# Kernel optimization log

Measured on AMD Instinct MI355X. Metric: run time of the kernel, lower is better.

## Reference

```python
import jax, jax.numpy as jnp
import numpy as np

B, FEAT, SPD_H, CTRL_H, N_CMD = 32768, 512, 128, 256, 4


def _p(key, shape, fan_in):
    # torch nn.Linear default init: U(-1/sqrt(fan_in), 1/sqrt(fan_in))
    lim = 1.0 / np.sqrt(fan_in)
    return jax.random.uniform(key, shape, jnp.float32, -lim, lim)


def setup_inputs() -> dict:
    key = jax.random.key(0)
    ks = iter(jax.random.split(key, 32))
    inp = {
        "feat": jax.random.normal(next(ks), (B, FEAT), jnp.float32),
        "speed": jax.random.uniform(next(ks), (B,), jnp.float32),
        "command": jax.random.randint(next(ks), (B,), 0, N_CMD, jnp.int32),
        "ms_w1": _p(next(ks), (1, SPD_H), 1), "ms_b1": _p(next(ks), (SPD_H,), 1),
        "ms_w2": _p(next(ks), (SPD_H, SPD_H), SPD_H), "ms_b2": _p(next(ks), (SPD_H,), SPD_H),
        "ms_w3": _p(next(ks), (SPD_H, SPD_H), SPD_H), "ms_b3": _p(next(ks), (SPD_H,), SPD_H),
        # speed_pred_module: 512 -> 256 -> 256 -> 1
        "sp_w1": _p(next(ks), (FEAT, CTRL_H), FEAT), "sp_b1": _p(next(ks), (CTRL_H,), FEAT),
        "sp_w2": _p(next(ks), (CTRL_H, CTRL_H), CTRL_H), "sp_b2": _p(next(ks), (CTRL_H,), CTRL_H),
        "sp_w3": _p(next(ks), (CTRL_H, 1), CTRL_H), "sp_b3": _p(next(ks), (1,), CTRL_H),
        # join_module: Linear(640, 512)
        "join_w": _p(next(ks), (FEAT + SPD_H, FEAT), FEAT + SPD_H),
        "join_b": _p(next(ks), (FEAT,), FEAT + SPD_H),
        # 4 control heads: 512 -> 256 -> 256 -> 3 (stacked on expert axis e)
        "ctrl_w1": _p(next(ks), (N_CMD, FEAT, CTRL_H), FEAT), "ctrl_b1": _p(next(ks), (N_CMD, CTRL_H), FEAT),
        "ctrl_w2": _p(next(ks), (N_CMD, CTRL_H, CTRL_H), CTRL_H), "ctrl_b2": _p(next(ks), (N_CMD, CTRL_H), CTRL_H),
        "ctrl_w3": _p(next(ks), (N_CMD, CTRL_H, 3), CTRL_H), "ctrl_b3": _p(next(ks), (N_CMD, 3), CTRL_H),
    }
    return inp


def _mlp(x, w1, b1, w2, b2, w3, b3):
    # FullyConnectedNet: Linear, ReLU, Linear, Dropout(p=0 -> noop), ReLU, Linear
    h = jax.nn.relu(x @ w1 + b1)
    h = jax.nn.relu(h @ w2 + b2)
    return h @ w3 + b3


def reference(feat, speed, command,
              ms_w1, ms_b1, ms_w2, ms_b2, ms_w3, ms_b3,
              sp_w1, sp_b1, sp_w2, sp_b2, sp_w3, sp_b3,
              join_w, join_b,
              ctrl_w1, ctrl_b1, ctrl_w2, ctrl_b2, ctrl_w3, ctrl_b3):
    v = _mlp(speed[:, None], ms_w1, ms_b1, ms_w2, ms_b2, ms_w3, ms_b3)      # [B,128]
    joined = jnp.concatenate([feat, v], axis=1) @ join_w + join_b           # [B,512]
    v_p = _mlp(feat, sp_w1, sp_b1, sp_w2, sp_b2, sp_w3, sp_b3)              # [B,1]
    # command-indexed dispatch: compute all 4 heads densely, then select per sample
    h1 = jax.nn.relu(jnp.einsum('bd,edh->beh', joined, ctrl_w1) + ctrl_b1)  # [B,4,256]
    h2 = jax.nn.relu(jnp.einsum('beh,ehk->bek', h1, ctrl_w2) + ctrl_b2)     # [B,4,256]
    act_all = jnp.einsum('bek,eko->beo', h2, ctrl_w3) + ctrl_b3             # [B,4,3]
    action = jnp.take_along_axis(act_all, command[:, None, None].astype(jnp.int32), axis=1)[:, 0]  # [B,3]
    throttle = jax.nn.sigmoid(action[:, 0])
    steering = jnp.tanh(action[:, 1])
    brake = jax.nn.sigmoid(action[:, 2])
    return v_p, throttle, brake, steering
```

## Files before the change

### kernel.cpp

```cpp
#include <hip/hip_runtime.h>
#include <hip/hip_bf16.h>
#include <stdint.h>
#include <math.h>

#define BB 32768
#define FEAT 512
#define SPD_H 128
#define CTRL_H 256
#define NCMD 4

typedef __attribute__((ext_vector_type(8))) short bf16x8;
typedef __attribute__((ext_vector_type(4))) float f32x4;

__device__ __forceinline__ unsigned short f2bf(float f) {
  union { float f; uint32_t u; } v; v.f = f;
  uint32_t u = v.u;
  return (unsigned short)((u + 0x7fffu + ((u >> 16) & 1u)) >> 16);
}

__device__ __forceinline__ void async16(const unsigned short* g, unsigned short* l) {
  __builtin_amdgcn_global_load_lds(
      (const __attribute__((address_space(1))) unsigned int*)g,
      (__attribute__((address_space(3))) unsigned int*)l, 16, 0, 0);
}

__device__ __forceinline__ void gemm128(
    const unsigned short* __restrict__ A, int lda,
    const int* __restrict__ perm, int m_start, int m_cnt,
    const unsigned short* __restrict__ W, const float* __restrict__ bi,
    unsigned short* __restrict__ C, int ldc, int relu, int K, int mt, int nt) {
  extern __shared__ __align__(16) unsigned char dynsm[];
  unsigned short* As = (unsigned short*)dynsm;
  unsigned short* Bs = As + 128 * 32;

  const int m0 = mt * 128;
  if (m0 >= m_cnt) return;
  const int n0 = nt * 128;
  const int t = threadIdx.x;
  const int w = t >> 6, lane = t & 63;
  const int wm = w & 1, wn = w >> 1;

  f32x4 acc[4][4];
#pragma unroll
  for (int i = 0; i < 4; ++i)
#pragma unroll
    for (int j = 0; j < 4; ++j)
#pragma unroll
      for (int r = 0; r < 4; ++r) acc[i][j][r] = 0.f;

  const int fr = lane & 15;
  const int fk = (lane >> 4) * 8;

  const unsigned short* agp[2]; const unsigned short* bgp[2];
  unsigned short* al[2]; unsigned short* bl[2];
#pragma unroll
  for (int it = 0; it < 2; ++it) {
    int row = w * 32 + it * 16 + (lane >> 2);
    int seg8 = (lane & 3) * 8;
    int rl = m0 + row;
    if (rl >= m_cnt) rl = m_cnt - 1;
    int grow = perm ? perm[m_start + rl] : (m_start + rl);
    agp[it] = A + (size_t)grow * lda + seg8;
    bgp[it] = W + (size_t)(n0 + row) * K + seg8;
    al[it] = As + (w * 32 + it * 16) * 32;
    bl[it] = Bs + (w * 32 + it * 16) * 32;
  }

  for (int k0 = 0; k0 < K; k0 += 32) {
#pragma unroll
    for (int it = 0; it < 2; ++it) {
      async16(agp[it] + k0, al[it]);
      async16(bgp[it] + k0, bl[it]);
    }
    __syncthreads();
    bf16x8 af[4], bfv[4];
#pragma unroll
    for (int i = 0; i < 4; ++i)
      af[i] = *(const bf16x8*)(As + (wm * 64 + i * 16 + fr) * 32 + fk);
#pragma unroll
    for (int j = 0; j < 4; ++j)
      bfv[j] = *(const bf16x8*)(Bs + (wn * 64 + j * 16 + fr) * 32 + fk);
#pragma unroll
    for (int i = 0; i < 4; ++i)
#pragma unroll
      for (int j = 0; j < 4; ++j)
        acc[i][j] = __builtin_amdgcn_mfma_f32_16x16x32_bf16(af[i], bfv[j], acc[i][j], 0, 0, 0);
    __syncthreads();
  }

  const int rquad = (lane >> 4) * 4;
  const int cidx = lane & 15;

  float bv[4];
#pragma unroll
  for (int j = 0; j < 4; ++j) bv[j] = bi ? bi[n0 + wn * 64 + j * 16 + cidx] : 0.f;

  unsigned short (*bscr)[136] = (unsigned short(*)[136])dynsm;
#pragma unroll
  for (int c = 0; c < 4; ++c) {
    if (wm == (c >> 1)) {
#pragma unroll
      for (int j = 0; j < 4; ++j) {
#pragma unroll
        for (int ii = 0; ii < 2; ++ii) {
          int i = 2 * (c & 1) + ii;
          int lr = ii * 16 + rquad;
#pragma unroll
          for (int r = 0; r < 4; ++r) {
            float v = acc[i][j][r] + bv[j];
            if (relu) v = fmaxf(v, 0.f);
            bscr[lr + r][wn * 64 + j * 16 + cidx] = f2bf(v);
          }
        }
      }
    }
    __syncthreads();
#pragma unroll
    for (int q = 0; q < 2; ++q) {
      int sg = t + 256 * q;
      int lr = sg >> 4, cs = (sg & 15) * 8;
      int grow = m0 + c * 32 + lr;
      if (grow < m_cnt)
        *(bf16x8*)(C + (size_t)(m_start + grow) * ldc + (n0 + cs)) =
            *(const bf16x8*)(&bscr[lr][cs]);
    }
    __syncthreads();
  }
}

struct WSeg { const float* src; unsigned short* dst; int K; int N; int ldd; };
struct PrepArgs {
  WSeg s[12];
  int start[13];
  const float* join_w; unsigned short* wjbf;
  const float* feat; unsigned short* ajoin;
  const int* cmd; int* wavecnt;
  const float* join_b; const float* ctrl_w1; const float* ctrl_b1; float* b_f;
};
__launch_bounds__(256)
__global__ void k_prep(PrepArgs a) {
  int bx = blockIdx.x, t = threadIdx.x;
  if (bx < 16384) {
    int idx = bx * 256 + t;
    int i = idx >> 7;
    int j4 = (idx & 127) << 2;
    float4 f = *(const float4*)(a.feat + (size_t)i * FEAT + j4);
    ushort4 o;
    o.x = f2bf(f.x); o.y = f2bf(f.y); o.z = f2bf(f.z); o.w = f2bf(f.w);
    *(ushort4*)(a.ajoin + (size_t)i * 640 + j4) = o;
    return;
  }
  int rel = bx - 16384;
  if (rel < 320) {
    int idx = rel * 256 + t;
    float4 f = *(const float4*)(a.join_w + (size_t)idx * 4);
    ushort4 o;
    o.x = f2bf(f.x); o.y = f2bf(f.y); o.z = f2bf(f.z); o.w = f2bf(f.w);
    *(ushort4*)(a.wjbf + (size_t)idx * 4) = o;
    return;
  }
  rel -= 320;
  if (rel < a.start[12]) {
    __shared__ float tb[32][33];
    int si = 0;
    while (rel >= a.start[si + 1]) ++si;
    WSeg sg = a.s[si];
    int tile = rel - a.start[si];
    int tkx = sg.K >> 5;
    int tn = tile / tkx;
    int tk = tile - tn * tkx;
    int k0 = tk * 32, n0 = tn * 32;
    int tx = t & 31, ty = t >> 5;
#pragma unroll
    for (int j = 0; j < 4; ++j)
      tb[ty + j * 8][tx] = sg.src[(size_t)(k0 + ty + j * 8) * sg.N + n0 + tx];
    __syncthreads();
#pragma unroll
    for (int j = 0; j < 4; ++j)
      sg.dst[(size_t)(n0 + ty + j * 8) * sg.ldd + k0 + tx] = f2bf(tb[tx][ty + j * 8]);
    return;
  }
  rel -= a.start[12];
  if (rel < 128) {
    int i = rel * 256 + t;
    int c = a.cmd[i];
    int wid = i >> 6;
    int lane = t & 63;
#pragma unroll
    for (int cv = 0; cv < NCMD; ++cv) {
      unsigned long long m = __ballot(c == cv);
      if (lane == 0) a.wavecnt[cv * 512 + wid] = __popcll(m);
    }
    return;
  }
  int e = rel - 128;
  float s0 = a.ctrl_b1[e * 256 + t], s1 = 0.f, s2 = 0.f, s3 = 0.f;
  const float* w = a.ctrl_w1 + (size_t)e * 512 * 256 + t;
#pragma unroll 4
  for (int m = 0; m < 512; m += 4) {
    s0 = fmaf(a.join_b[m + 0], w[(size_t)(m + 0) * 256], s0);
    s1 = fmaf(a.join_b[m + 1], w[(size_t)(m + 1) * 256], s1);
    s2 = fmaf(a.join_b[m + 2], w[(size_t)(m + 2) * 256], s2);
    s3 = fmaf(a.join_b[m + 3], w[(size_t)(m + 3) * 256], s3);
  }
  a.b_f[e * 256 + t] = (s0 + s1) + (s2 + s3);
}

struct MidArgs {
  const int* cmd; const int* wavecnt; int* perm; int* offs;
  const unsigned short* c_w1t; const unsigned short* wjbf; unsigned short* wf_t;
  const float* speed;
  const float* ms_w1; const float* ms_b1;
  const unsigned short* ms_w2t; const float* ms_b2;
  const unsigned short* ms_w3t; const float* ms_b3;
  unsigned short* ajoin;
  int* tile_e; int* tile_r0; int* ntl;
};
__launch_bounds__(256)
__global__ void k_mid(MidArgs a) {
  int b = blockIdx.x, t = threadIdx.x;
  if (b >= 168) {
    extern __shared__ __align__(16) unsigned char dynsm[];
    unsigned short (*hw)[136] = (unsigned short(*)[136])dynsm;
    unsigned short* BsM = (unsigned short*)(dynsm + 128 * 136 * 2);
    const int m0 = (b - 168) * 128;
    const int w = t >> 6, lane = t & 63;
    const int wm = w & 1, wn = w >> 1;
    const int fr = lane & 15, fk = (lane >> 4) * 8;
    const int rquad = (lane >> 4) * 4, cidx = lane & 15;
    {
      int r = t >> 1, half = t & 1;
      float s = a.speed[m0 + r];
#pragma unroll
      for (int c0 = 0; c0 < 64; c0 += 4) {
        int c = half * 64 + c0;
        float4 wv = *(const float4*)(a.ms_w1 + c);
        float4 bv = *(const float4*)(a.ms_b1 + c);
        hw[r][c + 0] = f2bf(fmaxf(fmaf(s, wv.x, bv.x), 0.f));
        hw[r][c + 1] = f2bf(fmaxf(fmaf(s, wv.y, bv.y), 0.f));
        hw[r][c + 2] = f2bf(fmaxf(fmaf(s, wv.z, bv.z), 0.f));
        hw[r][c + 3] = f2bf(fmaxf(fmaf(s, wv.w, bv.w), 0.f));
      }
    }
    __syncthreads();
    for (int layer = 0; layer < 2; ++layer) {
      const unsigned short* Wt = layer ? a.ms_w3t : a.ms_w2t;
      const float* bb = layer ? a.ms_b3 : a.ms_b2;
      f32x4 acc[4][4];
#pragma unroll
      for (int i = 0; i < 4; ++i)
#pragma unroll
        for (int j = 0; j < 4; ++j)
#pragma unroll
          for (int r = 0; r < 4; ++r) acc[i][j][r] = 0.f;
      for (int k0 = 0; k0 < 128; k0 += 32) {
#pragma unroll
        for (int it = 0; it < 2; ++it) {
          int row = w * 32 + it * 16 + (lane >> 2);
          async16(Wt + (size_t)row * 128 + k0 + (lane & 3) * 8,
                  BsM + (w * 32 + it * 16) * 32);
        }
        __syncthreads();
        bf16x8 af[4], bfv[4];
#pragma unroll
        for (int i = 0; i < 4; ++i)
          af[i] = *(const bf16x8*)(&hw[wm * 64 + i * 16 + fr][k0 + fk]);
#pragma unroll
        for (int j = 0; j < 4; ++j)
          bfv[j] = *(const bf16x8*)(BsM + (wn * 64 + j * 16 + fr) * 32 + fk);
#pragma unroll
        for (int i = 0; i < 4; ++i)
#pragma unroll
          for (int j = 0; j < 4; ++j)
            acc[i][j] = __builtin_amdgcn_mfma_f32_16x16x32_bf16(af[i], bfv[j], acc[i][j], 0, 0, 0);
        __syncthreads();
      }
#pragma unroll
      for (int j = 0; j < 4; ++j) {
        int col = wn * 64 + j * 16 + cidx;
        float bv = bb[col];
#pragma unroll
        for (int i = 0; i < 4; ++i) {
          int row = wm * 64 + i * 16 + rquad;
#pragma unroll
          for (int r = 0; r < 4; ++r) {
            float v = acc[i][j][r] + bv;
            if (layer == 0) v = fmaxf(v, 0.f);
            hw[row + r][col] = f2bf(v);
          }
        }
      }
      __syncthreads();
    }
    {
      int r = t >> 1, half = t & 1;
#pragma unroll
      for (int c8 = 0; c8 < 8; ++c8)
        *(bf16x8*)(a.ajoin + (size_t)(m0 + r) * 640 + 512 + half * 64 + c8 * 8) =
            *(const bf16x8*)(&hw[r][half * 64 + c8 * 8]);
    }
    return;
  }
  if (b >= 128) {
    int idx = b - 128;
    int mt = idx & 7, nt = idx >> 3;
    gemm128(a.c_w1t, 512, nullptr, 0, 1024, a.wjbf, nullptr, a.wf_t, 640, 0, 512, mt, nt);
    return;
  }
  __shared__ int pf[NCMD][4];
  __shared__ int tot[NCMD];
  int c = t >> 6, lane = t & 63;
  int v[8]; int s = 0;
#pragma unroll
  for (int q = 0; q < 8; ++q) { v[q] = a.wavecnt[c * 512 + lane * 8 + q]; s += v[q]; }
  int p = s;
#pragma unroll
  for (int m = 1; m < 64; m <<= 1) { int o = __shfl_up(p, m, 64); if (lane >= m) p += o; }
  int excl = p - s;
  if (lane == 63) tot[c] = p;
  if (lane == ((4 * b) >> 3)) {
    int base_off = (4 * b) & 7;
    int run = excl;
#pragma unroll
    for (int q = 0; q < 8; ++q) {
      if (q >= base_off && q < base_off + 4) pf[c][q - base_off] = run;
      run += v[q];
    }
  }
  __syncthreads();
  int soffs[NCMD + 1];
  soffs[0] = 0;
#pragma unroll
  for (int e = 0; e < NCMD; ++e) soffs[e + 1] = soffs[e] + tot[e];
  if (b == 0 && t == 0)
    for (int e = 0; e <= NCMD; ++e) a.offs[e] = soffs[e];
  int i = b * 256 + t;
  int mc = a.cmd[i];
  int lwid = t >> 6;
  int rank = 0, base = 0;
#pragma unroll
  for (int cv = 0; cv < NCMD; ++cv) {
    unsigned long long m = __ballot(mc == cv);
    if (mc == cv) {
      rank = __popcll(m & ((1ull << lane) - 1ull));
      base = soffs[cv] + pf[cv][lwid];
    }
  }
  a.perm[base + rank] = i;

  if (b == 0) {
    int toff[NCMD + 1];
    toff[0] = 0;
#pragma unroll
    for (int ee = 0; ee < NCMD; ++ee) toff[ee + 1] = toff[ee] + ((tot[ee] + 63) >> 6);
    if (t == 0) a.ntl[0] = toff[NCMD];
    for (int ti = t; ti < toff[NCMD]; ti += 256) {
      int ee = 0;
      while (ti >= toff[ee + 1]) ++ee;
      a.tile_e[ti] = ee;
      a.tile_r0[ti] = soffs[ee] + (ti - toff[ee]) * 64;
    }
  }
}

struct TailArgs {
  const unsigned short* ajoin;
  const unsigned short* wf_t;  const float* b_f;
  const unsigned short* sp_w1t; const float* sp_b1;
  const unsigned short* c_w2t; const float* ctrl_b2;
  const unsigned short* sp_w2t; const float* sp_b2;
  const float* ctrl_w3; const float* ctrl_b3;
  const float* sp_w3; const float* sp_b3;
  const int* perm; const int* seg;
  const int* tile_e; const int* tile_r0; const int* ntl;
  float* out;
};
__launch_bounds__(256, 3)
__global__ void k_tail(TailArgs a) {
  extern __shared__ __align__(16) unsigned char dynsm[];
  unsigned short* As = (unsigned short*)dynsm;
  unsigned short* h1 = (unsigned short*)(dynsm + 16384);
  float* pscr = (float*)dynsm;

  const int t = threadIdx.x;
  const int w = t >> 6, lane = t & 63;
  const int fr = lane & 15, fcg = lane >> 4;
  const int rquad = fcg * 4, cidx = fr;
  const int fkS = ((fcg ^ (fr & 3)) << 3);

  int is_sp, e = 0, NC;
  const unsigned short *W1, *W2;
  const float *b1, *b2;
  int r0, rend;
  if (blockIdx.x < 512) {
    is_sp = 1; NC = 8;
    W1 = a.sp_w1t; W2 = a.sp_w2t; b1 = a.sp_b1; b2 = a.sp_b2;
    r0 = blockIdx.x * 64; rend = BB;
  } else {
    int ti = blockIdx.x - 512;
    if (ti >= a.ntl[0]) return;
    is_sp = 0; e = a.tile_e[ti]; NC = 10;
    W1 = a.wf_t + (size_t)e * 256 * 640;
    W2 = a.c_w2t + (size_t)e * 65536;
    b1 = a.b_f + e * 256; b2 = a.ctrl_b2 + e * 256;
    r0 = a.tile_r0[ti]; rend = a.seg[e + 1];
  }
  const int K = is_sp ? 512 : 640;

  const unsigned short* agp[2];
  {
    int rl = r0 + w * 16 + (lane >> 2);
    if (rl >= rend) rl = rend - 1;
    int grow = is_sp ? rl : a.perm[rl];
    const unsigned short* g0 =
        a.ajoin + (size_t)grow * 640 + (((lane & 3) ^ ((lane >> 2) & 3)) << 3);
    agp[0] = g0; agp[1] = g0 + 32;
  }
  unsigned short* alb0 = As + w * 16 * 32;
  unsigned short* alb1 = As + 2048 + w * 16 * 32;

  const unsigned short* bp[4];
#pragma unroll
  for (int j = 0; j < 4; ++j)
    bp[j] = W1 + (size_t)(w * 64 + j * 16 + fr) * K + fcg * 8;

  f32x4 acc[4][4];
#pragma unroll
  for (int i = 0; i < 4; ++i)
#pragma unroll
    for (int j = 0; j < 4; ++j)
#pragma unroll
      for (int r = 0; r < 4; ++r) acc[i][j][r] = 0.f;

  async16(agp[0], alb0);
  async16(agp[1], alb1);

  for (int c = 0; c < NC; ++c) {
    const int cur = (c & 1) * 4096;
    if (c + 1 < NC) {
      const int nb = ((c + 1) & 1) * 4096;
      async16(agp[0] + (c + 1) * 64, alb0 + nb);
      async16(agp[1] + (c + 1) * 64, alb1 + nb);
      asm volatile("s_waitcnt vmcnt(2)" ::: "memory");
    } else {
      asm volatile("s_waitcnt vmcnt(0)" ::: "memory");
    }
    __builtin_amdgcn_s_barrier();
#pragma unroll
    for (int ks = 0; ks < 2; ++ks) {
      const int k0 = c * 64 + ks * 32;
      bf16x8 af[4], bv[4];
#pragma unroll
      for (int i = 0; i < 4; ++i)
        af[i] = *(const bf16x8*)(As + cur + ks * 2048 + (i * 16 + fr) * 32 + fkS);
#pragma unroll
      for (int j = 0; j < 4; ++j)
        bv[j] = *(const bf16x8*)(bp[j] + k0);
#pragma unroll
      for (int i = 0; i < 4; ++i)
#pragma unroll
        for (int j = 0; j < 4; ++j)
          acc[i][j] = __builtin_amdgcn_mfma_f32_16x16x32_bf16(af[i], bv[j], acc[i][j], 0, 0, 0);
    }
    __builtin_amdgcn_s_barrier();
  }

#pragma unroll
  for (int j = 0; j < 4; ++j) {
    const int col = w * 64 + j * 16 + cidx;
    const float bj = b1[col];
    const int c8 = col >> 3, cl = col & 7;
#pragma unroll
    for (int i = 0; i < 4; ++i) {
#pragma unroll
      for (int r = 0; r < 4; ++r) {
        const int row = i * 16 + rquad + r;
        h1[(row << 8) + (((c8 ^ (row & 7)) << 3) | cl)] =
            f2bf(fmaxf(acc[i][j][r] + bj, 0.f));
      }
    }
  }
  __syncthreads();

  const unsigned short* bp2[4];
#pragma unroll
  for (int j = 0; j < 4; ++j)
    bp2[j] = W2 + (size_t)(w * 64 + j * 16 + fr) * 256 + fcg * 8;

#pragma unroll
  for (int i = 0; i < 4; ++i)
#pragma unroll
    for (int j = 0; j < 4; ++j)
#pragma unroll
      for (int r = 0; r < 4; ++r) acc[i][j][r] = 0.f;

#pragma unroll 2
  for (int k0 = 0; k0 < 256; k0 += 32) {
    bf16x8 af[4], bv[4];
#pragma unroll
    for (int i = 0; i < 4; ++i) {
      const int row = i * 16 + fr;
      const int c8 = (k0 >> 3) + fcg;
      af[i] = *(const bf16x8*)(h1 + (row << 8) + ((c8 ^ (row & 7)) << 3));
    }
#pragma unroll
    for (int j = 0; j < 4; ++j)
      bv[j] = *(const bf16x8*)(bp2[j] + k0);
#pragma unroll
    for (int i = 0; i < 4; ++i)
#pragma unroll
      for (int j = 0; j < 4; ++j)
        acc[i][j] = __builtin_amdgcn_mfma_f32_16x16x32_bf16(af[i], bv[j], acc[i][j], 0, 0, 0);
  }

  float b2v[4], w30[4], w31[4], w32[4];
#pragma unroll
  for (int j = 0; j < 4; ++j) {
    const int col = w * 64 + j * 16 + cidx;
    b2v[j] = b2[col];
    if (is_sp) {
      w30[j] = a.sp_w3[col]; w31[j] = 0.f; w32[j] = 0.f;
    } else {
      const float* wp = a.ctrl_w3 + (size_t)e * 768 + col * 3;
      w30[j] = wp[0]; w31[j] = wp[1]; w32[j] = wp[2];
    }
  }
#pragma unroll
  for (int i = 0; i < 4; ++i) {
#pragma unroll
    for (int r = 0; r < 4; ++r) {
      float s0 = 0.f, s1 = 0.f, s2 = 0.f;
#pragma unroll
      for (int j = 0; j < 4; ++j) {
        const float v = fmaxf(acc[i][j][r] + b2v[j], 0.f);
        s0 = fmaf(v, w30[j], s0);
        if (!is_sp) { s1 = fmaf(v, w31[j], s1); s2 = fmaf(v, w32[j], s2); }
      }
#pragma unroll
      for (int m = 1; m <= 8; m <<= 1) {
        s0 += __shfl_xor(s0, m, 64);
        if (!is_sp) { s1 += __shfl_xor(s1, m, 64); s2 += __shfl_xor(s2, m, 64); }
      }
      if (cidx == 0) {
        const int row = i * 16 + rquad + r;
        pscr[(row * 4 + w) * 3 + 0] = s0;
        if (!is_sp) {
          pscr[(row * 4 + w) * 3 + 1] = s1;
          pscr[(row * 4 + w) * 3 + 2] = s2;
        }
      }
    }
  }
  __syncthreads();

  if (is_sp) {
    if (t < 64) {
      float s = pscr[t * 12] + pscr[t * 12 + 3] + pscr[t * 12 + 6] + pscr[t * 12 + 9]
              + a.sp_b3[0];
      a.out[r0 + t] = s;
    }
  } else {
    if (t < 192) {
      const int row = t / 3, o = t - row * 3;
      const int rl = r0 + row;
      if (rl < rend) {
        float s = pscr[row * 12 + o] + pscr[row * 12 + 3 + o] +
                  pscr[row * 12 + 6 + o] + pscr[row * 12 + 9 + o] +
                  a.ctrl_b3[e * 3 + o];
        const int orig = a.perm[rl];
        if (o == 0)      a.out[BB + orig]     = 1.f / (1.f + __expf(-s));
        else if (o == 2) a.out[2 * BB + orig] = 1.f / (1.f + __expf(-s));
        else             a.out[3 * BB + orig] = tanhf(s);
      }
    }
  }
}

static inline size_t align256(size_t x) { return (x + 255) & ~(size_t)255; }

extern "C" void kernel_launch(void* const* d_in, const int* in_sizes, int n_in,
                              void* d_out, int out_size, void* d_ws, size_t ws_size,
                              hipStream_t stream) {
  const float* feat   = (const float*)d_in[0];
  const float* speed  = (const float*)d_in[1];
  const int*   command= (const int*)d_in[2];
  const float* ms_w1  = (const float*)d_in[3];
  const float* ms_b1  = (const float*)d_in[4];
  const float* ms_w2  = (const float*)d_in[5];
  const float* ms_b2  = (const float*)d_in[6];
  const float* ms_w3  = (const float*)d_in[7];
  const float* ms_b3  = (const float*)d_in[8];
  const float* sp_w1  = (const float*)d_in[9];
  const float* sp_b1  = (const float*)d_in[10];
  const float* sp_w2  = (const float*)d_in[11];
  const float* sp_b2  = (const float*)d_in[12];
  const float* sp_w3  = (const float*)d_in[13];
  const float* sp_b3  = (const float*)d_in[14];
  const float* join_w = (const float*)d_in[15];
  const float* join_b = (const float*)d_in[16];
  const float* ctrl_w1= (const float*)d_in[17];
  const float* ctrl_b1= (const float*)d_in[18];
  const float* ctrl_w2= (const float*)d_in[19];
  const float* ctrl_b2= (const float*)d_in[20];
  const float* ctrl_w3= (const float*)d_in[21];
  const float* ctrl_b3= (const float*)d_in[22];
  float* out = (float*)d_out;

  char* ws = (char*)d_ws;
  size_t off = 0;
  auto alloc = [&](size_t bytes) -> char* { char* p = ws + off; off = align256(off + bytes); return p; };

  unsigned short* ajoin  = (unsigned short*)alloc((size_t)BB * 640 * 2);
  unsigned short* wtp    = (unsigned short*)alloc(1998848ull * 2);
  int* perm    = (int*)alloc((size_t)BB * 4);
  int* cnt     = (int*)alloc(64);
  int* wavecnt = (int*)alloc(4 * 512 * 4);
  float* b_f   = (float*)alloc(4 * 256 * 4);
  int* tile_e  = (int*)alloc(520 * 4);
  int* tile_r0 = (int*)alloc(520 * 4);
  int* ntl     = (int*)alloc(64);

  unsigned short* sp_w1t = wtp;
  unsigned short* sp_w2t = wtp + 131072;
  unsigned short* ms_w2t = wtp + 196608;
  unsigned short* ms_w3t = wtp + 212992;
  unsigned short* c_w1t  = wtp + 229376;
  unsigned short* c_w2t  = wtp + 753664;
  unsigned short* wjbf   = wtp + 1015808;
  unsigned short* wf_t   = wtp + 1343488;

  PrepArgs P;
  P.s[0] = { sp_w1, sp_w1t, 512, 256, 512 };
  P.s[1] = { sp_w2, sp_w2t, 256, 256, 256 };
  P.s[2] = { ms_w2, ms_w2t, 128, 128, 128 };
  P.s[3] = { ms_w3, ms_w3t, 128, 128, 128 };
  for (int e = 0; e < 4; ++e) P.s[4 + e] = { ctrl_w1 + (size_t)e * 512 * 256, c_w1t + (size_t)e * 131072, 512, 256, 512 };
  for (int e = 0; e < 4; ++e) P.s[8 + e] = { ctrl_w2 + (size_t)e * 256 * 256, c_w2t + (size_t)e * 65536, 256, 256, 256 };
  P.start[0] = 0;
  for (int i = 0; i < 12; ++i)
    P.start[i + 1] = P.start[i] + (P.s[i].K >> 5) * (P.s[i].N >> 5);
  P.join_w = join_w; P.wjbf = wjbf;
  P.feat = feat; P.ajoin = ajoin;
  P.cmd = command; P.wavecnt = wavecnt;
  P.join_b = join_b; P.ctrl_w1 = ctrl_w1; P.ctrl_b1 = ctrl_b1; P.b_f = b_f;
  int prep_blocks = 16384 + 320 + P.start[12] + 128 + 4;

  k_prep<<<prep_blocks, 256, 0, stream>>>(P);

  MidArgs Mi;
  Mi.cmd = command; Mi.wavecnt = wavecnt; Mi.perm = perm; Mi.offs = cnt + 4;
  Mi.c_w1t = c_w1t; Mi.wjbf = wjbf; Mi.wf_t = wf_t;
  Mi.speed = speed;
  Mi.ms_w1 = ms_w1; Mi.ms_b1 = ms_b1;
  Mi.ms_w2t = ms_w2t; Mi.ms_b2 = ms_b2;
  Mi.ms_w3t = ms_w3t; Mi.ms_b3 = ms_b3;
  Mi.ajoin = ajoin;
  Mi.tile_e = tile_e; Mi.tile_r0 = tile_r0; Mi.ntl = ntl;
  k_mid<<<168 + 256, 256, 128 * 136 * 2 + 128 * 32 * 2, stream>>>(Mi);

  TailArgs T;
  T.ajoin = ajoin; T.wf_t = wf_t; T.b_f = b_f;
  T.sp_w1t = sp_w1t; T.sp_b1 = sp_b1;
  T.c_w2t = c_w2t; T.ctrl_b2 = ctrl_b2;
  T.sp_w2t = sp_w2t; T.sp_b2 = sp_b2;
  T.ctrl_w3 = ctrl_w3; T.ctrl_b3 = ctrl_b3;
  T.sp_w3 = sp_w3; T.sp_b3 = sp_b3;
  T.perm = perm; T.seg = cnt + 4;
  T.tile_e = tile_e; T.tile_r0 = tile_r0; T.ntl = ntl;
  T.out = out;
  k_tail<<<dim3(512 + 516), 256, 49152, stream>>>(T);
}
```

Measured before the change: 240.7 us.

## Fuse speed-pred and control heads into one 512-thread tile sharing A loads

The tail kernel now runs both the speed-prediction MLP and the command-selected control head in the same 512-thread block. Waves 0-3 handle control and waves 4-7 handle speed-pred, and both consume one shared 64-wide swizzled A tile of permuted joined rows. This removes the separate 512 speed-pred blocks and their duplicate reads of the feature rows. Speed-pred outputs are scattered back through the permutation. The fused-bias precompute is also split across 32 blocks with partial sums, reduced by 4 extra blocks in the mid kernel, trading an extra pass for more parallelism. The cost is higher LDS use (80KB) and idle speed-pred waves during the extra K chunks.

```diff
diff --git a/kernel.cpp b/kernel.cpp
--- a/kernel.cpp
+++ b/kernel.cpp
@@ -135,7 +135,7 @@
   const float* join_w; unsigned short* wjbf;
   const float* feat; unsigned short* ajoin;
   const int* cmd; int* wavecnt;
-  const float* join_b; const float* ctrl_w1; const float* ctrl_b1; float* b_f;
+  const float* join_b; const float* ctrl_w1; float* bf_part;
 };
 __launch_bounds__(256)
 __global__ void k_prep(PrepArgs a) {
@@ -193,17 +193,25 @@
     }
     return;
   }
-  int e = rel - 128;
-  float s0 = a.ctrl_b1[e * 256 + t], s1 = 0.f, s2 = 0.f, s3 = 0.f;
-  const float* w = a.ctrl_w1 + (size_t)e * 512 * 256 + t;
-#pragma unroll 4
-  for (int m = 0; m < 512; m += 4) {
-    s0 = fmaf(a.join_b[m + 0], w[(size_t)(m + 0) * 256], s0);
-    s1 = fmaf(a.join_b[m + 1], w[(size_t)(m + 1) * 256], s1);
-    s2 = fmaf(a.join_b[m + 2], w[(size_t)(m + 2) * 256], s2);
-    s3 = fmaf(a.join_b[m + 3], w[(size_t)(m + 3) * 256], s3);
-  }
-  a.b_f[e * 256 + t] = (s0 + s1) + (s2 + s3);
+  int idx = rel - 128;
+  int e = idx >> 3, ch = idx & 7;
+  const float* w = a.ctrl_w1 + (size_t)e * 512 * 256 + (size_t)ch * 64 * 256 + t;
+  const float* jb = a.join_b + ch * 64;
+  float s0 = 0.f, s1 = 0.f, s2 = 0.f, s3 = 0.f;
+  float s4 = 0.f, s5 = 0.f, s6 = 0.f, s7 = 0.f;
+#pragma unroll
+  for (int g = 0; g < 8; ++g) {
+    s0 = fmaf(jb[g * 8 + 0], w[(size_t)(g * 8 + 0) * 256], s0);
+    s1 = fmaf(jb[g * 8 + 1], w[(size_t)(g * 8 + 1) * 256], s1);
+    s2 = fmaf(jb[g * 8 + 2], w[(size_t)(g * 8 + 2) * 256], s2);
+    s3 = fmaf(jb[g * 8 + 3], w[(size_t)(g * 8 + 3) * 256], s3);
+    s4 = fmaf(jb[g * 8 + 4], w[(size_t)(g * 8 + 4) * 256], s4);
+    s5 = fmaf(jb[g * 8 + 5], w[(size_t)(g * 8 + 5) * 256], s5);
+    s6 = fmaf(jb[g * 8 + 6], w[(size_t)(g * 8 + 6) * 256], s6);
+    s7 = fmaf(jb[g * 8 + 7], w[(size_t)(g * 8 + 7) * 256], s7);
+  }
+  a.bf_part[(size_t)(e * 8 + ch) * 256 + t] =
+      ((s0 + s1) + (s2 + s3)) + ((s4 + s5) + (s6 + s7));
 }
 
 struct MidArgs {
@@ -214,11 +222,20 @@
   const unsigned short* ms_w2t; const float* ms_b2;
   const unsigned short* ms_w3t; const float* ms_b3;
   unsigned short* ajoin;
+  const float* bf_part; const float* ctrl_b1; float* b_f;
   int* tile_e; int* tile_r0; int* ntl;
 };
 __launch_bounds__(256)
 __global__ void k_mid(MidArgs a) {
   int b = blockIdx.x, t = threadIdx.x;
+  if (b >= 424) {
+    int e = b - 424;
+    float s = a.ctrl_b1[e * 256 + t];
+#pragma unroll
+    for (int ch = 0; ch < 8; ++ch) s += a.bf_part[(size_t)(e * 8 + ch) * 256 + t];
+    a.b_f[e * 256 + t] = s;
+    return;
+  }
   if (b >= 168) {
     extern __shared__ __align__(16) unsigned char dynsm[];
     unsigned short (*hw)[136] = (unsigned short(*)[136])dynsm;
@@ -375,54 +392,51 @@
   const int* tile_e; const int* tile_r0; const int* ntl;
   float* out;
 };
-__launch_bounds__(256, 3)
+__launch_bounds__(512, 4)
 __global__ void k_tail(TailArgs a) {
   extern __shared__ __align__(16) unsigned char dynsm[];
-  unsigned short* As = (unsigned short*)dynsm;
-  unsigned short* h1 = (unsigned short*)(dynsm + 16384);
-  float* pscr = (float*)dynsm;
+  unsigned short* As  = (unsigned short*)dynsm;
+  unsigned short* h1c = (unsigned short*)(dynsm + 16384);
+  unsigned short* h1s = (unsigned short*)(dynsm + 49152);
+  float* pscr_c = (float*)dynsm;
+  float* pscr_s = (float*)(dynsm + 4096);
 
   const int t = threadIdx.x;
-  const int w = t >> 6, lane = t & 63;
+  const int wv = t >> 6, lane = t & 63;
   const int fr = lane & 15, fcg = lane >> 4;
   const int rquad = fcg * 4, cidx = fr;
-  const int fkS = ((fcg ^ (fr & 3)) << 3);
-
-  int is_sp, e = 0, NC;
-  const unsigned short *W1, *W2;
-  const float *b1, *b2;
-  int r0, rend;
-  if (blockIdx.x < 512) {
-    is_sp = 1; NC = 8;
-    W1 = a.sp_w1t; W2 = a.sp_w2t; b1 = a.sp_b1; b2 = a.sp_b2;
-    r0 = blockIdx.x * 64; rend = BB;
+
+  const int ti = blockIdx.x;
+  if (ti >= a.ntl[0]) return;
+  const int e = a.tile_e[ti];
+  const int r0 = a.tile_r0[ti], rend = a.seg[e + 1];
+
+  const bool is_sp = wv >= 4;
+  const int w = wv & 3;
+
+  int srow = r0 + wv * 8 + (lane >> 3);
+  if (srow >= rend) srow = rend - 1;
+  const unsigned short* asrc =
+      a.ajoin + (size_t)a.perm[srow] * 640 + (((lane & 7) ^ (lane >> 3)) << 3);
+  unsigned short* sdst = As + wv * 512;
+
+  const unsigned short* W1; const float* b1;
+  const unsigned short* W2; const float* b2;
+  unsigned short* h1;
+  int K1, NCm;
+  if (is_sp) {
+    W1 = a.sp_w1t; b1 = a.sp_b1; W2 = a.sp_w2t; b2 = a.sp_b2;
+    h1 = h1s; K1 = 512; NCm = 8;
   } else {
-    int ti = blockIdx.x - 512;
-    if (ti >= a.ntl[0]) return;
-    is_sp = 0; e = a.tile_e[ti]; NC = 10;
-    W1 = a.wf_t + (size_t)e * 256 * 640;
-    W2 = a.c_w2t + (size_t)e * 65536;
-    b1 = a.b_f + e * 256; b2 = a.ctrl_b2 + e * 256;
-    r0 = a.tile_r0[ti]; rend = a.seg[e + 1];
-  }
-  const int K = is_sp ? 512 : 640;
-
-  const unsigned short* agp[2];
-  {
-    int rl = r0 + w * 16 + (lane >> 2);
-    if (rl >= rend) rl = rend - 1;
-    int grow = is_sp ? rl : a.perm[rl];
-    const unsigned short* g0 =
-        a.ajoin + (size_t)grow * 640 + (((lane & 3) ^ ((lane >> 2) & 3)) << 3);
-    agp[0] = g0; agp[1] = g0 + 32;
-  }
-  unsigned short* alb0 = As + w * 16 * 32;
-  unsigned short* alb1 = As + 2048 + w * 16 * 32;
+    W1 = a.wf_t + (size_t)e * 256 * 640; b1 = a.b_f + e * 256;
+    W2 = a.c_w2t + (size_t)e * 65536; b2 = a.ctrl_b2 + e * 256;
+    h1 = h1c; K1 = 640; NCm = 10;
+  }
 
   const unsigned short* bp[4];
 #pragma unroll
   for (int j = 0; j < 4; ++j)
-    bp[j] = W1 + (size_t)(w * 64 + j * 16 + fr) * K + fcg * 8;
+    bp[j] = W1 + (size_t)(w * 64 + j * 16 + fr) * K1 + fcg * 8;
 
   f32x4 acc[4][4];
 #pragma unroll
@@ -432,37 +446,35 @@
 #pragma unroll
       for (int r = 0; r < 4; ++r) acc[i][j][r] = 0.f;
 
-  async16(agp[0], alb0);
-  async16(agp[1], alb1);
-
-  for (int c = 0; c < NC; ++c) {
-    const int cur = (c & 1) * 4096;
-    if (c + 1 < NC) {
-      const int nb = ((c + 1) & 1) * 4096;
-      async16(agp[0] + (c + 1) * 64, alb0 + nb);
-      async16(agp[1] + (c + 1) * 64, alb1 + nb);
-      asm volatile("s_waitcnt vmcnt(2)" ::: "memory");
-    } else {
-      asm volatile("s_waitcnt vmcnt(0)" ::: "memory");
-    }
-    __builtin_amdgcn_s_barrier();
-#pragma unroll
-    for (int ks = 0; ks < 2; ++ks) {
-      const int k0 = c * 64 + ks * 32;
-      bf16x8 af[4], bv[4];
-#pragma unroll
-      for (int i = 0; i < 4; ++i)
-        af[i] = *(const bf16x8*)(As + cur + ks * 2048 + (i * 16 + fr) * 32 + fkS);
-#pragma unroll
-      for (int j = 0; j < 4; ++j)
-        bv[j] = *(const bf16x8*)(bp[j] + k0);
-#pragma unroll
-      for (int i = 0; i < 4; ++i)
+  async16(asrc, sdst);
+  async16(asrc + 64, sdst + 4096);
+
+  for (int c = 0; c < 10; ++c) {
+    if (c < 9) asm volatile("s_waitcnt vmcnt(1)" ::: "memory");
+    else       asm volatile("s_waitcnt vmcnt(0)" ::: "memory");
+    asm volatile("s_barrier" ::: "memory");
+    if (c < NCm) {
+      const unsigned short* cbuf = As + (c & 1) * 4096;
+#pragma unroll
+      for (int ks = 0; ks < 2; ++ks) {
+        const int k0 = c * 64 + ks * 32;
+        bf16x8 af[4], bv[4];
+#pragma unroll
+        for (int i = 0; i < 4; ++i)
+          af[i] = *(const bf16x8*)(cbuf + (i * 16 + fr) * 64 +
+                                   (((ks * 4 + fcg) ^ (fr & 7)) << 3));
 #pragma unroll
         for (int j = 0; j < 4; ++j)
-          acc[i][j] = __builtin_amdgcn_mfma_f32_16x16x32_bf16(af[i], bv[j], acc[i][j], 0, 0, 0);
-    }
-    __builtin_amdgcn_s_barrier();
+          bv[j] = *(const bf16x8*)(bp[j] + k0);
+#pragma unroll
+        for (int i = 0; i < 4; ++i)
+#pragma unroll
+          for (int j = 0; j < 4; ++j)
+            acc[i][j] = __builtin_amdgcn_mfma_f32_16x16x32_bf16(af[i], bv[j], acc[i][j], 0, 0, 0);
+      }
+    }
+    asm volatile("s_barrier" ::: "memory");
+    if (c < 8) async16(asrc + (c + 2) * 64, sdst + (c & 1) * 4096);
   }
 
 #pragma unroll
@@ -543,35 +555,37 @@
       }
       if (cidx == 0) {
         const int row = i * 16 + rquad + r;
-        pscr[(row * 4 + w) * 3 + 0] = s0;
-        if (!is_sp) {
-          pscr[(row * 4 + w) * 3 + 1] = s1;
-          pscr[(row * 4 + w) * 3 + 2] = s2;
+        if (is_sp) {
+          pscr_s[row * 4 + w] = s0;
+        } else {
+          pscr_c[(row * 4 + w) * 3 + 0] = s0;
+          pscr_c[(row * 4 + w) * 3 + 1] = s1;
+          pscr_c[(row * 4 + w) * 3 + 2] = s2;
         }
       }
     }
   }
   __syncthreads();
 
-  if (is_sp) {
-    if (t < 64) {
-      float s = pscr[t * 12] + pscr[t * 12 + 3] + pscr[t * 12 + 6] + pscr[t * 12 + 9]
-              + a.sp_b3[0];
-      a.out[r0 + t] = s;
-    }
-  } else {
-    if (t < 192) {
-      const int row = t / 3, o = t - row * 3;
-      const int rl = r0 + row;
-      if (rl < rend) {
-        float s = pscr[row * 12 + o] + pscr[row * 12 + 3 + o] +
-                  pscr[row * 12 + 6 + o] + pscr[row * 12 + 9 + o] +
-                  a.ctrl_b3[e * 3 + o];
-        const int orig = a.perm[rl];
-        if (o == 0)      a.out[BB + orig]     = 1.f / (1.f + __expf(-s));
-        else if (o == 2) a.out[2 * BB + orig] = 1.f / (1.f + __expf(-s));
-        else             a.out[3 * BB + orig] = tanhf(s);
-      }
+  if (t < 64) {
+    const int rl = r0 + t;
+    if (rl < rend) {
+      float s = pscr_s[t * 4 + 0] + pscr_s[t * 4 + 1] +
+                pscr_s[t * 4 + 2] + pscr_s[t * 4 + 3] + a.sp_b3[0];
+      a.out[a.perm[rl]] = s;
+    }
+  }
+  if (t < 192) {
+    const int row = t / 3, o = t - row * 3;
+    const int rl = r0 + row;
+    if (rl < rend) {
+      float s = pscr_c[row * 12 + o] + pscr_c[row * 12 + 3 + o] +
+                pscr_c[row * 12 + 6 + o] + pscr_c[row * 12 + 9 + o] +
+                a.ctrl_b3[e * 3 + o];
+      const int orig = a.perm[rl];
+      if (o == 0)      a.out[BB + orig]     = 1.f / (1.f + __expf(-s));
+      else if (o == 2) a.out[2 * BB + orig] = 1.f / (1.f + __expf(-s));
+      else             a.out[3 * BB + orig] = tanhf(s);
     }
   }
 }
@@ -615,9 +629,10 @@
   int* perm    = (int*)alloc((size_t)BB * 4);
   int* cnt     = (int*)alloc(64);
   int* wavecnt = (int*)alloc(4 * 512 * 4);
+  float* bf_part = (float*)alloc(4 * 8 * 256 * 4);
   float* b_f   = (float*)alloc(4 * 256 * 4);
-  int* tile_e  = (int*)alloc(520 * 4);
-  int* tile_r0 = (int*)alloc(520 * 4);
+  int* tile_e  = (int*)alloc(1056 * 4);
+  int* tile_r0 = (int*)alloc(1056 * 4);
   int* ntl     = (int*)alloc(64);
 
   unsigned short* sp_w1t = wtp;
@@ -642,8 +657,8 @@
   P.join_w = join_w; P.wjbf = wjbf;
   P.feat = feat; P.ajoin = ajoin;
   P.cmd = command; P.wavecnt = wavecnt;
-  P.join_b = join_b; P.ctrl_w1 = ctrl_w1; P.ctrl_b1 = ctrl_b1; P.b_f = b_f;
-  int prep_blocks = 16384 + 320 + P.start[12] + 128 + 4;
+  P.join_b = join_b; P.ctrl_w1 = ctrl_w1; P.bf_part = bf_part;
+  int prep_blocks = 16384 + 320 + P.start[12] + 128 + 32;
 
   k_prep<<<prep_blocks, 256, 0, stream>>>(P);
 
@@ -655,11 +670,13 @@
   Mi.ms_w2t = ms_w2t; Mi.ms_b2 = ms_b2;
   Mi.ms_w3t = ms_w3t; Mi.ms_b3 = ms_b3;
   Mi.ajoin = ajoin;
+  Mi.bf_part = bf_part; Mi.ctrl_b1 = ctrl_b1; Mi.b_f = b_f;
   Mi.tile_e = tile_e; Mi.tile_r0 = tile_r0; Mi.ntl = ntl;
-  k_mid<<<168 + 256, 256, 128 * 136 * 2 + 128 * 32 * 2, stream>>>(Mi);
+  k_mid<<<168 + 256 + 4, 256, 128 * 136 * 2 + 128 * 32 * 2, stream>>>(Mi);
 
   TailArgs T;
-  T.ajoin = ajoin; T.wf_t = wf_t; T.b_f = b_f;
+  T.ajoin = ajoin;
+  T.wf_t = wf_t; T.b_f = b_f;
   T.sp_w1t = sp_w1t; T.sp_b1 = sp_b1;
   T.c_w2t = c_w2t; T.ctrl_b2 = ctrl_b2;
   T.sp_w2t = sp_w2t; T.sp_b2 = sp_b2;
@@ -668,5 +685,5 @@
   T.perm = perm; T.seg = cnt + 4;
   T.tile_e = tile_e; T.tile_r0 = tile_r0; T.ntl = ntl;
   T.out = out;
-  k_tail<<<dim3(512 + 516), 256, 49152, stream>>>(T);
+  k_tail<<<dim3(520), 512, 81920, stream>>>(T);
 }
```

Result: slower. 247.5 us (+2.8%).
